# Optimization experiments

Measured on AMD Instinct MI355X. Metric: run time of the kernel, lower is better.

Reference implementation:

```python
import jax, jax.numpy as jnp
import numpy as np

ROI_SIZE = 7
MAX_BIN_H = 8   # max adaptive-maxpool bin height for crop H <= 37
MAX_BIN_W = 9   # max adaptive-maxpool bin width  for crop W <= 50
SCALE = 0.0625  # 1/16 feature stride


def setup_inputs() -> dict:
    key = jax.random.key(0)
    ks = jax.random.split(key, 12)
    B, C, h, w = 1, 512, 37, 50          # conv5 feature map of a 600x800 image
    N = 512                               # number of ROIs (proposals)
    n_class = 21
    d_in, d_fc = C * ROI_SIZE * ROI_SIZE, 4096
    x = jax.random.normal(ks[0], (B, C, h, w), dtype=jnp.float32)
    # rois in image coordinates (x1, y1, x2, y2), image is 800x600
    x1 = jax.random.uniform(ks[1], (N,), minval=0.0, maxval=700.0)
    y1 = jax.random.uniform(ks[2], (N,), minval=0.0, maxval=500.0)
    bw = jax.random.uniform(ks[3], (N,), minval=16.0, maxval=400.0)
    bh = jax.random.uniform(ks[4], (N,), minval=16.0, maxval=300.0)
    rois = jnp.stack([x1, y1, jnp.minimum(x1 + bw, 799.0), jnp.minimum(y1 + bh, 599.0)], axis=1).astype(jnp.float32)
    roi_index = jnp.zeros((N,), dtype=jnp.int32)  # single image in batch
    W1 = jax.random.normal(ks[5], (d_in, d_fc), dtype=jnp.float32) * 0.01
    b1 = jnp.zeros((d_fc,), dtype=jnp.float32)
    W2 = jax.random.normal(ks[6], (d_fc, d_fc), dtype=jnp.float32) * 0.01
    b2 = jnp.zeros((d_fc,), dtype=jnp.float32)
    Wp = jax.random.normal(ks[7], (d_fc, n_class * 4), dtype=jnp.float32) * 0.001
    bp = jax.random.normal(ks[8], (n_class * 4,), dtype=jnp.float32) * 0.001
    Ws = jax.random.normal(ks[9], (d_fc, n_class), dtype=jnp.float32) * 0.01
    bs = jax.random.normal(ks[10], (n_class,), dtype=jnp.float32) * 0.01
    return dict(x=x, rois=rois, roi_index=roi_index, W1=W1, b1=b1, W2=W2, b2=b2, Wp=Wp, bp=bp, Ws=Ws, bs=bs)


def _roi_pool(x, rois, roi_index):
    """Faithful port of roi_pooling(): per-ROI crop + AdaptiveMaxPool2d(7)."""
    B, C, h, w = x.shape
    S = ROI_SIZE
    coords = jnp.round(rois * SCALE)  # round-half-even, like torch.round
    cx1 = jnp.clip(coords[:, 0], 0, w).astype(jnp.int32)
    cy1 = jnp.clip(coords[:, 1], 0, h).astype(jnp.int32)
    cx2 = jnp.clip(coords[:, 2], 0, w).astype(jnp.int32)
    cy2 = jnp.clip(coords[:, 3], 0, h).astype(jnp.int32)
    bidx = roi_index.astype(jnp.int32)
    roi_stack = jnp.stack([bidx, cx1, cy1, cx2, cy2], axis=1)  # [N,5]

    def pool_one(carry, roi):
        bi, x1i, y1i, x2i, y2i = roi[0], roi[1], roi[2], roi[3], roi[4]
        valid = (x1i < x2i) & (y1i < y2i)
        # torch slicing roi[2]:roi[4]+1 silently truncates at the tensor edge
        x2e = jnp.minimum(x2i, w - 1)
        y2e = jnp.minimum(y2i, h - 1)
        Hc = y2e - y1i + 1
        Wc = x2e - x1i + 1
        i = jnp.arange(S)
        # adaptive max pool bins: [floor(i*H/S), ceil((i+1)*H/S))
        rs = y1i + (i * Hc) // S
        re = y1i + ((i + 1) * Hc + S - 1) // S
        cs = x1i + (i * Wc) // S
        ce = x1i + ((i + 1) * Wc + S - 1) // S
        rows = rs[:, None] + jnp.arange(MAX_BIN_H)          # [S, MBH]
        rmask = rows < re[:, None]
        rows = jnp.clip(rows, 0, h - 1)
        cols = cs[:, None] + jnp.arange(MAX_BIN_W)          # [S, MBW]
        cmask = cols < ce[:, None]
        cols = jnp.clip(cols, 0, w - 1)
        feat = x[bi]                                         # [C, h, w]
        g = feat[:, rows[:, None, :, None], cols[None, :, None, :]]  # [C,S,S,MBH,MBW]
        mask = rmask[:, None, :, None] & cmask[None, :, None, :]     # [S,S,MBH,MBW]
        pooled = jnp.where(mask, g, -jnp.inf).max(axis=(-2, -1))    # [C,S,S]
        pooled = jnp.where(valid, pooled, jnp.zeros_like(pooled))
        return carry, pooled

    _, out = jax.lax.scan(pool_one, None, roi_stack)  # [N, C, S, S]
    return out


def reference(x, rois, roi_index, W1, b1, W2, b2, Wp, bp, Ws, bs):
    pooled = _roi_pool(x, rois, roi_index)            # [N, 512, 7, 7]
    flat = pooled.reshape(pooled.shape[0], -1)        # [N, 25088]
    fc6 = jax.nn.relu(flat @ W1 + b1)                 # [N, 4096]
    fc7 = jax.nn.relu(fc6 @ W2 + b2)                  # [N, 4096]
    roi_class_params = fc7 @ Wp + bp                  # [N, n_class*4]
    roi_scores = fc7 @ Ws + bs                        # [N, n_class]
    return (roi_class_params, roi_scores)
```

## Files before the change

### kernel.cpp

```cpp
#include <hip/hip_runtime.h>
#include <hip/hip_bf16.h>

using f32x4  = float          __attribute__((ext_vector_type(4)));
using bf16x8 = __bf16         __attribute__((ext_vector_type(8)));
using u16x8  = unsigned short __attribute__((ext_vector_type(8)));

#define C_CH 512
#define H_IN 37
#define W_IN 50
#define NPOS 1850
#define NROI 512
#define DIN  25088
#define DFC  4096
#define NPAR 84
#define NCLS 21
#define KS_FC 4
#define KS_HEAD 16

#define PB_X  232
#define PB_WH 2048
#define PB_TOT (PB_X + PB_WH)

__device__ __forceinline__ unsigned pack_bf16x2(float a, float b) {
    __hip_bfloat162 h;
    h.x = __float2bfloat16(a);
    h.y = __float2bfloat16(b);
    return *reinterpret_cast<unsigned*>(&h);
}

__global__ __launch_bounds__(256) void prep_kernel(
        const float* __restrict__ x, float* __restrict__ xt,
        const float* __restrict__ Wp, const float* __restrict__ Ws,
        float* __restrict__ Whp) {
    __shared__ float tile[64][65];
    int b = blockIdx.x;
    int t = threadIdx.x;
    if (b < PB_X) {
        int p0 = (b % 29) * 64;
        int c0 = (b / 29) * 64;
        int tc = t & 63, tr = t >> 6;
#pragma unroll
        for (int i = 0; i < 16; ++i) {
            int r = tr + i * 4;
            int p = p0 + tc;
            float v = 0.f;
            if (p < NPOS) v = x[(size_t)(c0 + r) * NPOS + p];
            tile[r][tc] = v;
        }
        __syncthreads();
#pragma unroll
        for (int i = 0; i < 16; ++i) {
            int rw = tr + i * 4;
            int p = p0 + rw;
            if (p < NPOS) xt[(size_t)p * C_CH + c0 + tc] = tile[tc][rw];
        }
    } else {
        int idx = (b - PB_X) * 256 + t;
        int k = idx >> 7, c = idx & 127;
        float v = 0.f;
        if (c < NPAR) v = Wp[(size_t)k * NPAR + c];
        else if (c < NPAR + NCLS) v = Ws[(size_t)k * NCLS + (c - NPAR)];
        Whp[idx] = v;
    }
}

__global__ __launch_bounds__(256) void roi_pool_kernel(
        const float* __restrict__ xt, const float* __restrict__ rois,
        __hip_bfloat16* __restrict__ pooled) {
    int n = blockIdx.x;
    int t = threadIdx.x;
    float4 rv = reinterpret_cast<const float4*>(rois)[n];
    int x1 = (int)fminf(fmaxf(rintf(rv.x * 0.0625f), 0.f), (float)W_IN);
    int y1 = (int)fminf(fmaxf(rintf(rv.y * 0.0625f), 0.f), (float)H_IN);
    int x2 = (int)fminf(fmaxf(rintf(rv.z * 0.0625f), 0.f), (float)W_IN);
    int y2 = (int)fminf(fmaxf(rintf(rv.w * 0.0625f), 0.f), (float)H_IN);
    bool valid = (x1 < x2) && (y1 < y2);
    unsigned* outp = reinterpret_cast<unsigned*>(pooled) + (size_t)n * (DIN / 2);
    if (!valid) {
        for (int b = 0; b < 49; ++b) outp[b * 256 + t] = 0u;
        return;
    }
    int x2e = min(x2, W_IN - 1), y2e = min(y2, H_IN - 1);
    int Hc = y2e - y1 + 1, Wc = x2e - x1 + 1;
    const float2* base = reinterpret_cast<const float2*>(xt);
    for (int i = 0; i < 7; ++i) {
        int rs = y1 + (i * Hc) / 7;
        int re = y1 + ((i + 1) * Hc + 6) / 7;
        for (int j = 0; j < 7; ++j) {
            int cs = x1 + (j * Wc) / 7;
            int ce = x1 + ((j + 1) * Wc + 6) / 7;
            float m0 = -__builtin_inff(), m1 = -__builtin_inff();
            for (int r = rs; r < re; ++r) {
                const float2* rowp = base + (size_t)r * (W_IN * C_CH / 2) + t;
                for (int c = cs; c < ce; ++c) {
                    float2 v = rowp[c * (C_CH / 2)];
                    m0 = fmaxf(m0, v.x);
                    m1 = fmaxf(m1, v.y);
                }
            }
            outp[(i * 7 + j) * 256 + t] = pack_bf16x2(m0, m1);
        }
    }
}

__device__ __forceinline__ void gload_lds16(const void* src, void* dst) {
    __builtin_amdgcn_global_load_lds(
        (const __attribute__((address_space(1))) void*)src,
        (__attribute__((address_space(3))) void*)dst, 16, 0, 0);
}

__global__ __launch_bounds__(256, 2) void gemm_f32b_kernel(
        const __hip_bfloat16* __restrict__ A,
        const float* __restrict__ Bf,
        float* __restrict__ Cp,
        int N, int lda, int ldbn, int kChunk, int nMT, int nNT, int Mtot,
        int perm) {
    __shared__ __align__(16) char lA[128 * 128];
    __shared__ __align__(16) char lB[128 * 128];
    int q = gridDim.x >> 3;
    int bid = (blockIdx.x & 7) * q + (blockIdx.x >> 3);
    int mt = bid % nMT;
    int nt = (bid / nMT) % nNT;
    int ks = bid / (nMT * nNT);
    int m0 = mt * 128, n0 = nt * 128;
    int k0 = ks * kChunk;
    int t = threadIdx.x;
    int lane = t & 63, wid = t >> 6;

    const char* srcA[4]; char* dstA[4];
#pragma unroll
    for (int i = 0; i < 4; ++i) {
        int chunk = i * 4 + wid;
        int p = chunk * 1024 + lane * 16;
        int row = p >> 7;
        int swz = ((row ^ (row >> 3)) & 7) << 4;
        srcA[i] = (const char*)A + ((size_t)(m0 + row) * lda + k0) * 2
                  + ((p & 127) ^ swz);
        dstA[i] = lA + chunk * 1024;
    }

    int n4 = (t & 31) * 4;
    int k8 = (t >> 5) * 8;
    int woff[4];
#pragma unroll
    for (int j = 0; j < 4; ++j) {
        int row = n4 + j;
        int swz = ((row ^ (row >> 3)) & 7) << 4;
        woff[j] = row * 128 + ((k8 * 2) ^ swz);
    }

    int wm = wid >> 1, wn = wid & 1;
    int kb0 = (lane >> 4) << 4;
    int roA[4], roB[4], sA[4], sB[4];
#pragma unroll
    for (int f = 0; f < 4; ++f) {
        int ra = wm * 64 + f * 16 + (lane & 15);
        int rb = wn * 64 + f * 16 + (lane & 15);
        roA[f] = ra * 128; sA[f] = ((ra ^ (ra >> 3)) & 7) << 4;
        roB[f] = rb * 128; sB[f] = ((rb ^ (rb >> 3)) & 7) << 4;
    }

    int nkt = kChunk >> 6;
    f32x4 acc[4][4] = {};
    f32x4 vA[8], vB[8];
    const float* Bbase = Bf + n0 + n4;

    auto loadB = [&](int kt, f32x4* v) {
        int kb = k0 + kt * 64;
        int rbase = perm ? ((kb & 511) * 49 + (kb >> 9)) : kb;
        int rstr  = perm ? 49 : 1;
#pragma unroll
        for (int p = 0; p < 8; ++p)
            v[p] = *reinterpret_cast<const f32x4*>(
                Bbase + (size_t)(rbase + (k8 + p) * rstr) * ldbn);
    };

    auto halfBody = [&](int kt, f32x4* v) {
#pragma unroll
        for (int i = 0; i < 4; ++i) { gload_lds16(srcA[i], dstA[i]); srcA[i] += 128; }
#pragma unroll
        for (int j = 0; j < 4; ++j) {
            uint4 w;
            w.x = pack_bf16x2(v[0][j], v[1][j]);
            w.y = pack_bf16x2(v[2][j], v[3][j]);
            w.z = pack_bf16x2(v[4][j], v[5][j]);
            w.w = pack_bf16x2(v[6][j], v[7][j]);
            *reinterpret_cast<uint4*>(lB + woff[j]) = w;
        }
        if (kt + 2 < nkt) {
            loadB(kt + 2, v);
            asm volatile("s_waitcnt vmcnt(8) lgkmcnt(0)\ns_barrier" ::: "memory");
        } else {
            asm volatile("s_waitcnt vmcnt(0) lgkmcnt(0)\ns_barrier" ::: "memory");
        }
#pragma unroll
        for (int ksub = 0; ksub < 2; ++ksub) {
            int kk = kb0 | (ksub << 6);
            bf16x8 af[4], bfr[4];
#pragma unroll
            for (int f = 0; f < 4; ++f)
                af[f] = *reinterpret_cast<const bf16x8*>(lA + roA[f] + (kk ^ sA[f]));
#pragma unroll
            for (int f = 0; f < 4; ++f)
                bfr[f] = *reinterpret_cast<const bf16x8*>(lB + roB[f] + (kk ^ sB[f]));
#pragma unroll
            for (int mf = 0; mf < 4; ++mf)
#pragma unroll
                for (int nf = 0; nf < 4; ++nf)
                    acc[mf][nf] = __builtin_amdgcn_mfma_f32_16x16x32_bf16(
                        af[mf], bfr[nf], acc[mf][nf], 0, 0, 0);
        }
        asm volatile("s_barrier" ::: "memory");
    };

    loadB(0, vA);
    if (nkt > 1) loadB(1, vB);
    for (int kt = 0; kt + 1 < nkt; kt += 2) {
        halfBody(kt, vA);
        halfBody(kt + 1, vB);
    }
    if (nkt & 1) halfBody(nkt - 1, vA);

    float* outp = Cp + (size_t)ks * Mtot * N;
    int rbase = m0 + wm * 64;
    int cbase = n0 + wn * 64 + (lane & 15);
    int rl = (lane >> 4) * 4;
#pragma unroll
    for (int mf = 0; mf < 4; ++mf)
#pragma unroll
        for (int nf = 0; nf < 4; ++nf)
#pragma unroll
            for (int r = 0; r < 4; ++r)
                outp[(size_t)(rbase + mf * 16 + rl + r) * N + cbase + nf * 16] =
                    acc[mf][nf][r];
}

__global__ __launch_bounds__(256) void reduce_bias_relu_kernel(
        const float* __restrict__ P, const float* __restrict__ bias,
        __hip_bfloat16* __restrict__ out, int MN, int N, int KS) {
    int idx = blockIdx.x * blockDim.x + threadIdx.x;
    int e0 = idx * 4;
    if (e0 >= MN) return;
    f32x4 s = *reinterpret_cast<const f32x4*>(P + e0);
    for (int k = 1; k < KS; ++k)
        s += *reinterpret_cast<const f32x4*>(P + (size_t)k * MN + e0);
    f32x4 b = *reinterpret_cast<const f32x4*>(bias + (e0 & (N - 1)));
    s += b;
    uint2 pk;
    pk.x = pack_bf16x2(fmaxf(s[0], 0.f), fmaxf(s[1], 0.f));
    pk.y = pack_bf16x2(fmaxf(s[2], 0.f), fmaxf(s[3], 0.f));
    *reinterpret_cast<uint2*>(reinterpret_cast<char*>(out) + (size_t)e0 * 2) = pk;
}

__global__ __launch_bounds__(128) void head_reduce_kernel(
        const float* __restrict__ P, const float* __restrict__ bp,
        const float* __restrict__ bs, float* __restrict__ out) {
    int n = blockIdx.x, c = threadIdx.x;
    float s = 0.f;
#pragma unroll
    for (int ks = 0; ks < KS_HEAD; ++ks)
        s += P[(size_t)ks * NROI * 128 + (size_t)n * 128 + c];
    if (c < NPAR)
        out[(size_t)n * NPAR + c] = s + bp[c];
    else if (c < NPAR + NCLS)
        out[(size_t)NROI * NPAR + (size_t)n * NCLS + (c - NPAR)] = s + bs[c - NPAR];
}

extern "C" void kernel_launch(void* const* d_in, const int* in_sizes, int n_in,
                              void* d_out, int out_size, void* d_ws, size_t ws_size,
                              hipStream_t stream) {
    const float* x    = (const float*)d_in[0];
    const float* rois = (const float*)d_in[1];
    const float* W1 = (const float*)d_in[3];
    const float* b1 = (const float*)d_in[4];
    const float* W2 = (const float*)d_in[5];
    const float* b2 = (const float*)d_in[6];
    const float* Wp = (const float*)d_in[7];
    const float* bp = (const float*)d_in[8];
    const float* Ws = (const float*)d_in[9];
    const float* bs = (const float*)d_in[10];
    float* out = (float*)d_out;

    const size_t MB = 1ull << 20;
    char* ws = (char*)d_ws;
    float*          xt     = (float*)(ws + 0);
    __hip_bfloat16* pooled = (__hip_bfloat16*)(ws + 4   * MB);
    float*          Whp    = (float*)(ws + 30  * MB);
    float*          part   = (float*)(ws + 34  * MB);
    __hip_bfloat16* fc6    = (__hip_bfloat16*)(ws + 104 * MB);
    __hip_bfloat16* fc7    = (__hip_bfloat16*)(ws + 109 * MB);

    prep_kernel<<<PB_TOT, 256, 0, stream>>>(x, xt, Wp, Ws, Whp);
    roi_pool_kernel<<<NROI, 256, 0, stream>>>(xt, rois, pooled);

    gemm_f32b_kernel<<<4 * 32 * KS_FC, 256, 0, stream>>>(
        pooled, W1, part, DFC, DIN, DFC, DIN / KS_FC, 4, 32, NROI, 1);
    reduce_bias_relu_kernel<<<2048, 256, 0, stream>>>(part, b1, fc6,
                                                      NROI * DFC, DFC, KS_FC);

    gemm_f32b_kernel<<<4 * 32 * KS_FC, 256, 0, stream>>>(
        fc6, W2, part, DFC, DFC, DFC, DFC / KS_FC, 4, 32, NROI, 0);
    reduce_bias_relu_kernel<<<2048, 256, 0, stream>>>(part, b2, fc7,
                                                      NROI * DFC, DFC, KS_FC);

    gemm_f32b_kernel<<<4 * KS_HEAD, 256, 0, stream>>>(fc7, Whp, part,
                                                      128, DFC, 128, DFC / KS_HEAD,
                                                      4, 1, NROI, 0);
    head_reduce_kernel<<<NROI, 128, 0, stream>>>(part, bp, bs, out);
}
```

Measured before the change: 407.2 us.

## Triple-buffer A and double-buffer B in LDS for the FC GEMM

Restructures the GEMM main loop so A tiles are loaded into a 3-deep LDS ring and converted B tiles into a 2-deep LDS ring. Each iteration issues the next A prefetch, runs MFMAs on the current buffers, and converts and writes the next B tile. This leaves one barrier per k-step instead of two. The goal is to overlap global loads and the fp32-to-bf16 conversion with MFMA compute. In exchange LDS use rises from 32KB to 80KB per block, which may lower occupancy below the 2 blocks per CU that launch_bounds asks for.

```diff
diff --git a/kernel.cpp b/kernel.cpp
--- a/kernel.cpp
+++ b/kernel.cpp
@@ -115,8 +115,8 @@
         float* __restrict__ Cp,
         int N, int lda, int ldbn, int kChunk, int nMT, int nNT, int Mtot,
         int perm) {
-    __shared__ __align__(16) char lA[128 * 128];
-    __shared__ __align__(16) char lB[128 * 128];
+    __shared__ __align__(16) char lA[3 * 16384];
+    __shared__ __align__(16) char lB[2 * 16384];
     int q = gridDim.x >> 3;
     int bid = (blockIdx.x & 7) * q + (blockIdx.x >> 3);
     int mt = bid % nMT;
@@ -127,7 +127,7 @@
     int t = threadIdx.x;
     int lane = t & 63, wid = t >> 6;
 
-    const char* srcA[4]; char* dstA[4];
+    const char* srcA[4]; int offA[4];
 #pragma unroll
     for (int i = 0; i < 4; ++i) {
         int chunk = i * 4 + wid;
@@ -136,8 +136,15 @@
         int swz = ((row ^ (row >> 3)) & 7) << 4;
         srcA[i] = (const char*)A + ((size_t)(m0 + row) * lda + k0) * 2
                   + ((p & 127) ^ swz);
-        dstA[i] = lA + chunk * 1024;
-    }
+        offA[i] = chunk * 1024;
+    }
+    auto stageA = [&](int buf) {
+#pragma unroll
+        for (int i = 0; i < 4; ++i) {
+            gload_lds16(srcA[i], lA + buf * 16384 + offA[i]);
+            srcA[i] += 128;
+        }
+    };
 
     int n4 = (t & 31) * 4;
     int k8 = (t >> 5) * 8;
@@ -148,24 +155,9 @@
         int swz = ((row ^ (row >> 3)) & 7) << 4;
         woff[j] = row * 128 + ((k8 * 2) ^ swz);
     }
-
-    int wm = wid >> 1, wn = wid & 1;
-    int kb0 = (lane >> 4) << 4;
-    int roA[4], roB[4], sA[4], sB[4];
-#pragma unroll
-    for (int f = 0; f < 4; ++f) {
-        int ra = wm * 64 + f * 16 + (lane & 15);
-        int rb = wn * 64 + f * 16 + (lane & 15);
-        roA[f] = ra * 128; sA[f] = ((ra ^ (ra >> 3)) & 7) << 4;
-        roB[f] = rb * 128; sB[f] = ((rb ^ (rb >> 3)) & 7) << 4;
-    }
-
-    int nkt = kChunk >> 6;
-    f32x4 acc[4][4] = {};
-    f32x4 vA[8], vB[8];
     const float* Bbase = Bf + n0 + n4;
-
-    auto loadB = [&](int kt, f32x4* v) {
+    f32x4 v[8];
+    auto loadB = [&](int kt) {
         int kb = k0 + kt * 64;
         int rbase = perm ? ((kb & 511) * 49 + (kb >> 9)) : kb;
         int rstr  = perm ? 49 : 1;
@@ -174,10 +166,7 @@
             v[p] = *reinterpret_cast<const f32x4*>(
                 Bbase + (size_t)(rbase + (k8 + p) * rstr) * ldbn);
     };
-
-    auto halfBody = [&](int kt, f32x4* v) {
-#pragma unroll
-        for (int i = 0; i < 4; ++i) { gload_lds16(srcA[i], dstA[i]); srcA[i] += 128; }
+    auto cvtB = [&](int buf) {
 #pragma unroll
         for (int j = 0; j < 4; ++j) {
             uint4 w;
@@ -185,24 +174,35 @@
             w.y = pack_bf16x2(v[2][j], v[3][j]);
             w.z = pack_bf16x2(v[4][j], v[5][j]);
             w.w = pack_bf16x2(v[6][j], v[7][j]);
-            *reinterpret_cast<uint4*>(lB + woff[j]) = w;
-        }
-        if (kt + 2 < nkt) {
-            loadB(kt + 2, v);
-            asm volatile("s_waitcnt vmcnt(8) lgkmcnt(0)\ns_barrier" ::: "memory");
-        } else {
-            asm volatile("s_waitcnt vmcnt(0) lgkmcnt(0)\ns_barrier" ::: "memory");
-        }
+            *reinterpret_cast<uint4*>(lB + buf * 16384 + woff[j]) = w;
+        }
+    };
+
+    int wm = wid >> 1, wn = wid & 1;
+    int kb0 = (lane >> 4) << 4;
+    int roA[4], roB[4], sA[4], sB[4];
+#pragma unroll
+    for (int f = 0; f < 4; ++f) {
+        int ra = wm * 64 + f * 16 + (lane & 15);
+        int rb = wn * 64 + f * 16 + (lane & 15);
+        roA[f] = ra * 128; sA[f] = ((ra ^ (ra >> 3)) & 7) << 4;
+        roB[f] = rb * 128; sB[f] = ((rb ^ (rb >> 3)) & 7) << 4;
+    }
+
+    f32x4 acc[4][4] = {};
+    auto mfmaStep = [&](int aBuf, int bBuf) {
+        const char* baseA = lA + aBuf * 16384;
+        const char* baseB = lB + bBuf * 16384;
 #pragma unroll
         for (int ksub = 0; ksub < 2; ++ksub) {
             int kk = kb0 | (ksub << 6);
             bf16x8 af[4], bfr[4];
 #pragma unroll
             for (int f = 0; f < 4; ++f)
-                af[f] = *reinterpret_cast<const bf16x8*>(lA + roA[f] + (kk ^ sA[f]));
+                af[f] = *reinterpret_cast<const bf16x8*>(baseA + roA[f] + (kk ^ sA[f]));
 #pragma unroll
             for (int f = 0; f < 4; ++f)
-                bfr[f] = *reinterpret_cast<const bf16x8*>(lB + roB[f] + (kk ^ sB[f]));
+                bfr[f] = *reinterpret_cast<const bf16x8*>(baseB + roB[f] + (kk ^ sB[f]));
 #pragma unroll
             for (int mf = 0; mf < 4; ++mf)
 #pragma unroll
@@ -210,16 +210,34 @@
                     acc[mf][nf] = __builtin_amdgcn_mfma_f32_16x16x32_bf16(
                         af[mf], bfr[nf], acc[mf][nf], 0, 0, 0);
         }
-        asm volatile("s_barrier" ::: "memory");
     };
 
-    loadB(0, vA);
-    if (nkt > 1) loadB(1, vB);
-    for (int kt = 0; kt + 1 < nkt; kt += 2) {
-        halfBody(kt, vA);
-        halfBody(kt + 1, vB);
-    }
-    if (nkt & 1) halfBody(nkt - 1, vA);
+    int nkt = kChunk >> 6;
+
+    stageA(0);
+    stageA(1);
+    loadB(0);
+    cvtB(0);
+    loadB(1);
+    asm volatile("s_waitcnt vmcnt(8) lgkmcnt(0)\ns_barrier" ::: "memory");
+
+    int aCur = 0, aStage = 2, bCur = 0;
+    for (int kt = 0; kt + 2 < nkt; ++kt) {
+        stageA(aStage);
+        mfmaStep(aCur, bCur);
+        cvtB(bCur ^ 1);
+        loadB(kt + 2);
+        asm volatile("s_waitcnt vmcnt(12) lgkmcnt(0)\ns_barrier" ::: "memory");
+        aCur = aCur == 2 ? 0 : aCur + 1;
+        aStage = aStage == 2 ? 0 : aStage + 1;
+        bCur ^= 1;
+    }
+    mfmaStep(aCur, bCur);
+    cvtB(bCur ^ 1);
+    asm volatile("s_waitcnt vmcnt(0) lgkmcnt(0)\ns_barrier" ::: "memory");
+    aCur = aCur == 2 ? 0 : aCur + 1;
+    bCur ^= 1;
+    mfmaStep(aCur, bCur);
 
     float* outp = Cp + (size_t)ks * Mtot * N;
     int rbase = m0 + wm * 64;
```

Measured after the change: 369.5 us, median of 2. -9.3%, faster.

## Triple-buffer A and double-buffer B in LDS with single barrier per k-step

Applied to the files above, without the earlier changes.

Restructures the GEMM main loop so A tiles are staged into three rotating LDS buffers and converted B tiles into two, allowing each k-step to issue loads for future tiles, run MFMAs on the current tile and convert the next B tile with only one barrier. MFMA sections get raised wave priority. Split-K counts change (fc7 to 8, head to 8), and the head reduce now takes KS as a runtime argument. The loop is unrolled by 6 and assumes nkt-2 is a multiple of 6; LDS use rises to 80KB per block, which may reduce occupancy below the requested 2 blocks per CU.

```diff
diff --git a/kernel.cpp b/kernel.cpp
--- a/kernel.cpp
+++ b/kernel.cpp
@@ -14,8 +14,9 @@
 #define DFC  4096
 #define NPAR 84
 #define NCLS 21
-#define KS_FC 4
-#define KS_HEAD 16
+#define KS1   4
+#define KS2   8
+#define KSH   8
 
 #define PB_X  232
 #define PB_WH 2048
@@ -115,8 +116,12 @@
         float* __restrict__ Cp,
         int N, int lda, int ldbn, int kChunk, int nMT, int nNT, int Mtot,
         int perm) {
-    __shared__ __align__(16) char lA[128 * 128];
-    __shared__ __align__(16) char lB[128 * 128];
+    __shared__ __align__(16) char lA0[16384];
+    __shared__ __align__(16) char lA1[16384];
+    __shared__ __align__(16) char lA2[16384];
+    __shared__ __align__(16) char lB0[16384];
+    __shared__ __align__(16) char lB1[16384];
+
     int q = gridDim.x >> 3;
     int bid = (blockIdx.x & 7) * q + (blockIdx.x >> 3);
     int mt = bid % nMT;
@@ -127,7 +132,7 @@
     int t = threadIdx.x;
     int lane = t & 63, wid = t >> 6;
 
-    const char* srcA[4]; char* dstA[4];
+    const char* srcA[4]; int offA[4];
 #pragma unroll
     for (int i = 0; i < 4; ++i) {
         int chunk = i * 4 + wid;
@@ -136,11 +141,23 @@
         int swz = ((row ^ (row >> 3)) & 7) << 4;
         srcA[i] = (const char*)A + ((size_t)(m0 + row) * lda + k0) * 2
                   + ((p & 127) ^ swz);
-        dstA[i] = lA + chunk * 1024;
-    }
+        offA[i] = chunk * 1024;
+    }
+    auto stageA = [&](char* buf) {
+#pragma unroll
+        for (int i = 0; i < 4; ++i) {
+            gload_lds16(srcA[i], buf + offA[i]);
+            srcA[i] += 128;
+        }
+    };
 
     int n4 = (t & 31) * 4;
     int k8 = (t >> 5) * 8;
+    int rstr = perm ? 49 : 1;
+    const float* pB = Bf + n0 + n4;
+    int koff[8];
+#pragma unroll
+    for (int p = 0; p < 8; ++p) koff[p] = (k8 + p) * rstr * ldbn;
     int woff[4];
 #pragma unroll
     for (int j = 0; j < 4; ++j) {
@@ -148,36 +165,15 @@
         int swz = ((row ^ (row >> 3)) & 7) << 4;
         woff[j] = row * 128 + ((k8 * 2) ^ swz);
     }
-
-    int wm = wid >> 1, wn = wid & 1;
-    int kb0 = (lane >> 4) << 4;
-    int roA[4], roB[4], sA[4], sB[4];
-#pragma unroll
-    for (int f = 0; f < 4; ++f) {
-        int ra = wm * 64 + f * 16 + (lane & 15);
-        int rb = wn * 64 + f * 16 + (lane & 15);
-        roA[f] = ra * 128; sA[f] = ((ra ^ (ra >> 3)) & 7) << 4;
-        roB[f] = rb * 128; sB[f] = ((rb ^ (rb >> 3)) & 7) << 4;
-    }
-
-    int nkt = kChunk >> 6;
-    f32x4 acc[4][4] = {};
-    f32x4 vA[8], vB[8];
-    const float* Bbase = Bf + n0 + n4;
-
-    auto loadB = [&](int kt, f32x4* v) {
-        int kb = k0 + kt * 64;
-        int rbase = perm ? ((kb & 511) * 49 + (kb >> 9)) : kb;
-        int rstr  = perm ? 49 : 1;
+    auto loadB = [&](int kt, f32x4 (&v)[8]) {
+        int kb = k0 + (kt << 6);
+        int rb = perm ? ((kb & 511) * 49 + (kb >> 9)) : kb;
+        int rbo = rb * ldbn;
 #pragma unroll
         for (int p = 0; p < 8; ++p)
-            v[p] = *reinterpret_cast<const f32x4*>(
-                Bbase + (size_t)(rbase + (k8 + p) * rstr) * ldbn);
-    };
-
-    auto halfBody = [&](int kt, f32x4* v) {
-#pragma unroll
-        for (int i = 0; i < 4; ++i) { gload_lds16(srcA[i], dstA[i]); srcA[i] += 128; }
+            v[p] = *reinterpret_cast<const f32x4*>(pB + (size_t)(rbo + koff[p]));
+    };
+    auto cvtB = [&](f32x4 (&v)[8], char* bW) {
 #pragma unroll
         for (int j = 0; j < 4; ++j) {
             uint4 w;
@@ -185,24 +181,34 @@
             w.y = pack_bf16x2(v[2][j], v[3][j]);
             w.z = pack_bf16x2(v[4][j], v[5][j]);
             w.w = pack_bf16x2(v[6][j], v[7][j]);
-            *reinterpret_cast<uint4*>(lB + woff[j]) = w;
-        }
-        if (kt + 2 < nkt) {
-            loadB(kt + 2, v);
-            asm volatile("s_waitcnt vmcnt(8) lgkmcnt(0)\ns_barrier" ::: "memory");
-        } else {
-            asm volatile("s_waitcnt vmcnt(0) lgkmcnt(0)\ns_barrier" ::: "memory");
-        }
+            *reinterpret_cast<uint4*>(bW + woff[j]) = w;
+        }
+    };
+
+    int wm = wid >> 1, wn = wid & 1;
+    int kb0 = (lane >> 4) << 4;
+    int roA[4], roB[4], sA[4], sB[4];
+#pragma unroll
+    for (int f = 0; f < 4; ++f) {
+        int ra = wm * 64 + f * 16 + (lane & 15);
+        int rb = wn * 64 + f * 16 + (lane & 15);
+        roA[f] = ra * 128; sA[f] = ((ra ^ (ra >> 3)) & 7) << 4;
+        roB[f] = rb * 128; sB[f] = ((rb ^ (rb >> 3)) & 7) << 4;
+    }
+
+    f32x4 acc[4][4] = {};
+    auto mfmaStep = [&](const char* bA, const char* bB) {
+        __builtin_amdgcn_s_setprio(1);
 #pragma unroll
         for (int ksub = 0; ksub < 2; ++ksub) {
             int kk = kb0 | (ksub << 6);
             bf16x8 af[4], bfr[4];
 #pragma unroll
             for (int f = 0; f < 4; ++f)
-                af[f] = *reinterpret_cast<const bf16x8*>(lA + roA[f] + (kk ^ sA[f]));
+                af[f] = *reinterpret_cast<const bf16x8*>(bA + roA[f] + (kk ^ sA[f]));
 #pragma unroll
             for (int f = 0; f < 4; ++f)
-                bfr[f] = *reinterpret_cast<const bf16x8*>(lB + roB[f] + (kk ^ sB[f]));
+                bfr[f] = *reinterpret_cast<const bf16x8*>(bB + roB[f] + (kk ^ sB[f]));
 #pragma unroll
             for (int mf = 0; mf < 4; ++mf)
 #pragma unroll
@@ -210,16 +216,40 @@
                     acc[mf][nf] = __builtin_amdgcn_mfma_f32_16x16x32_bf16(
                         af[mf], bfr[nf], acc[mf][nf], 0, 0, 0);
         }
-        asm volatile("s_barrier" ::: "memory");
-    };
-
-    loadB(0, vA);
-    if (nkt > 1) loadB(1, vB);
-    for (int kt = 0; kt + 1 < nkt; kt += 2) {
-        halfBody(kt, vA);
-        halfBody(kt + 1, vB);
-    }
-    if (nkt & 1) halfBody(nkt - 1, vA);
+        __builtin_amdgcn_s_setprio(0);
+    };
+
+    f32x4 sP[8], sQ[8];
+    auto body = [&](int kt, char* aR, char* aS,
+                    f32x4 (&vC)[8], f32x4 (&vL)[8], char* bR, char* bW) {
+        stageA(aS);
+        loadB(kt + 2, vL);
+        mfmaStep(aR, bR);
+        cvtB(vC, bW);
+        asm volatile("s_waitcnt lgkmcnt(0)\ns_barrier" ::: "memory");
+    };
+
+    int nkt = kChunk >> 6;
+
+    stageA(lA0);
+    stageA(lA1);
+    loadB(0, sP);
+    loadB(1, sQ);
+    cvtB(sP, lB0);
+    asm volatile("s_waitcnt lgkmcnt(0)\ns_barrier" ::: "memory");
+
+    for (int kt = 0; kt + 2 < nkt; kt += 6) {
+        body(kt + 0, lA0, lA2, sQ, sP, lB0, lB1);
+        body(kt + 1, lA1, lA0, sP, sQ, lB1, lB0);
+        body(kt + 2, lA2, lA1, sQ, sP, lB0, lB1);
+        body(kt + 3, lA0, lA2, sP, sQ, lB1, lB0);
+        body(kt + 4, lA1, lA0, sQ, sP, lB0, lB1);
+        body(kt + 5, lA2, lA1, sP, sQ, lB1, lB0);
+    }
+    mfmaStep(lA0, lB0);
+    cvtB(sQ, lB1);
+    asm volatile("s_waitcnt vmcnt(0) lgkmcnt(0)\ns_barrier" ::: "memory");
+    mfmaStep(lA1, lB1);
 
     float* outp = Cp + (size_t)ks * Mtot * N;
     int rbase = m0 + wm * 64;
@@ -254,11 +284,10 @@
 
 __global__ __launch_bounds__(128) void head_reduce_kernel(
         const float* __restrict__ P, const float* __restrict__ bp,
-        const float* __restrict__ bs, float* __restrict__ out) {
+        const float* __restrict__ bs, float* __restrict__ out, int KS) {
     int n = blockIdx.x, c = threadIdx.x;
     float s = 0.f;
-#pragma unroll
-    for (int ks = 0; ks < KS_HEAD; ++ks)
+    for (int ks = 0; ks < KS; ++ks)
         s += P[(size_t)ks * NROI * 128 + (size_t)n * 128 + c];
     if (c < NPAR)
         out[(size_t)n * NPAR + c] = s + bp[c];
@@ -293,18 +322,18 @@
     prep_kernel<<<PB_TOT, 256, 0, stream>>>(x, xt, Wp, Ws, Whp);
     roi_pool_kernel<<<NROI, 256, 0, stream>>>(xt, rois, pooled);
 
-    gemm_f32b_kernel<<<4 * 32 * KS_FC, 256, 0, stream>>>(
-        pooled, W1, part, DFC, DIN, DFC, DIN / KS_FC, 4, 32, NROI, 1);
+    gemm_f32b_kernel<<<4 * 32 * KS1, 256, 0, stream>>>(
+        pooled, W1, part, DFC, DIN, DFC, DIN / KS1, 4, 32, NROI, 1);
     reduce_bias_relu_kernel<<<2048, 256, 0, stream>>>(part, b1, fc6,
-                                                      NROI * DFC, DFC, KS_FC);
-
-    gemm_f32b_kernel<<<4 * 32 * KS_FC, 256, 0, stream>>>(
-        fc6, W2, part, DFC, DFC, DFC, DFC / KS_FC, 4, 32, NROI, 0);
+                                                      NROI * DFC, DFC, KS1);
+
+    gemm_f32b_kernel<<<4 * 32 * KS2, 256, 0, stream>>>(
+        fc6, W2, part, DFC, DFC, DFC, DFC / KS2, 4, 32, NROI, 0);
     reduce_bias_relu_kernel<<<2048, 256, 0, stream>>>(part, b2, fc7,
-                                                      NROI * DFC, DFC, KS_FC);
-
-    gemm_f32b_kernel<<<4 * KS_HEAD, 256, 0, stream>>>(fc7, Whp, part,
-                                                      128, DFC, 128, DFC / KS_HEAD,
-                                                      4, 1, NROI, 0);
-    head_reduce_kernel<<<NROI, 128, 0, stream>>>(part, bp, bs, out);
-}
+                                                      NROI * DFC, DFC, KS2);
+
+    gemm_f32b_kernel<<<4 * KSH, 256, 0, stream>>>(fc7, Whp, part,
+                                                  128, DFC, 128, DFC / KSH,
+                                                  4, 1, NROI, 0);
+    head_reduce_kernel<<<NROI, 128, 0, stream>>>(part, bp, bs, out, KSH);
+}
```

Result: no change. 410.6 us (+0.8%).
